# Kernel optimization log

Hardware: AMD Instinct MI355X
Metric: run time of the kernel (lower is better)

Reference implementation:

```python
import jax, jax.numpy as jnp
import numpy as np

B, N, H, NH = 2, 1024, 1024, 16  # batch, seq per branch, hidden, heads


def setup_inputs() -> dict:
    key = jax.random.key(0)
    k1, k2, k3, k4 = jax.random.split(key, 4)
    x = jax.random.normal(k1, (B, N, H), jnp.float32)
    x2 = jax.random.normal(k2, (B, N, H), jnp.float32)
    w_qkv = jax.random.normal(k3, (3 * H, H), jnp.float32) * 0.02  # nn.Linear(H, 3H), no bias
    w_out = jax.random.normal(k4, (H, H), jnp.float32) * 0.02
    b_out = jnp.zeros((H,), jnp.float32)
    return {"x": x, "x2": x2, "w_qkv": w_qkv, "w_out": w_out, "b_out": b_out, "num_heads": NH}


def _qkv_split(x, w_qkv, nh):
    # qkv Linear then Rearrange 'b n (qkv l d) -> qkv b l n d'
    b, n, h = x.shape
    d = h // nh
    qkv = x @ w_qkv.T                                    # [b, n, 3h]
    qkv = qkv.reshape(b, n, 3, nh, d).transpose(2, 0, 3, 1, 4)  # [3, b, nh, n, d]
    return qkv[0], qkv[1], qkv[2]


def reference(x, x2, w_qkv, w_out, b_out, num_heads):
    nh = num_heads
    d = x.shape[-1] // nh
    scale = float(d) ** -0.5
    q, k, v = _qkv_split(x, w_qkv, nh)
    q2, k2, v2 = _qkv_split(x2, w_qkv, nh)
    # cross-branch concat along seq dim
    q = jnp.concatenate([q, q2], axis=2)
    k = jnp.concatenate([k, k2], axis=2)
    v = jnp.concatenate([v, v2], axis=2)
    att = jax.nn.softmax(jnp.einsum('bhxd,bhyd->bhxy', q, k) * scale, axis=-1)  # [b,nh,2N,2N]
    o = jnp.einsum('bhxy,bhyd->bhxd', att, v)            # [b,nh,2N,d]
    o1, o2 = jnp.split(o, 2, axis=2)

    def proj(o):
        b, h, n, dd = o.shape
        o = o.transpose(0, 2, 1, 3).reshape(b, n, h * dd)  # 'b h l d -> b l (h d)'
        return o @ w_out.T + b_out

    return proj(o1), proj(o2)
```

## Files before the change

kernel.cpp:

```cpp
#include <hip/hip_runtime.h>
#include <hip/hip_bf16.h>

#define NB      2
#define NSEQ    1024
#define S2      2048
#define HDIM    1024
#define NHEADS  16
#define DHEAD   64
#define Q_SCALE 0.18033688011112042f

typedef unsigned short ushort_t;
typedef __attribute__((ext_vector_type(8))) short short8;
typedef __attribute__((ext_vector_type(4))) float f32x4;

__device__ __forceinline__ ushort_t f2bf(float f) {
    union { float f; unsigned int u; } c; c.f = f;
    unsigned int u = c.u;
    u += 0x7FFFu + ((u >> 16) & 1u);
    return (ushort_t)(u >> 16);
}

__device__ __forceinline__ unsigned pack_bf16x2(float a, float b) {
    union { __hip_bfloat162 h; unsigned u; } cv;
    cv.h = __float22bfloat162_rn(float2{a, b});
    return cv.u;
}

__global__ __launch_bounds__(256) void cvt_all(
    const float* __restrict__ x, const float* __restrict__ x2,
    const float* __restrict__ wqkv, const float* __restrict__ wout,
    ushort_t* __restrict__ Xb, ushort_t* __restrict__ Wqb, ushort_t* __restrict__ Wob)
{
    int b = blockIdx.x;
    const float* s; ushort_t* d; int i;
    if (b < 2048)      { s = x;    d = Xb;            i = b * 256 + threadIdx.x; }
    else if (b < 4096) { s = x2;   d = Xb + 2097152;  i = (b - 2048) * 256 + threadIdx.x; }
    else if (b < 7168) { s = wqkv; d = Wqb;           i = (b - 4096) * 256 + threadIdx.x; }
    else               { s = wout; d = Wob;           i = (b - 7168) * 256 + threadIdx.x; }
    float4 v = ((const float4*)s)[i];
    ushort4 o; o.x = f2bf(v.x); o.y = f2bf(v.y); o.z = f2bf(v.z); o.w = f2bf(v.w);
    ((ushort4*)d)[i] = o;
}

__global__ __launch_bounds__(256) void qkv_gemm_mfma(
    const ushort_t* __restrict__ Xb, const ushort_t* __restrict__ Wqb,
    ushort_t* __restrict__ Qb, ushort_t* __restrict__ Kb, ushort_t* __restrict__ Vtb)
{
    __shared__ ushort_t As[128 * 32];
    __shared__ ushort_t Bs[128 * 32];
    __shared__ float    Sc[4][16 * 20];
    const int t = threadIdx.x;
    const int lane = t & 63, quad = lane >> 4, l15 = lane & 15;
    const int w = t >> 6;
    const int wm = (w >> 1) * 64, wn = (w & 1) * 64;
    const int r0 = blockIdx.y * 128, c0 = blockIdx.x * 128;

    const int g_chunk = (lane & 3) ^ ((lane >> 3) & 3);
    const int srow_lo = w * 16 + (lane >> 2);

    f32x4 acc[4][4];
    #pragma unroll
    for (int i = 0; i < 4; ++i)
        #pragma unroll
        for (int j = 0; j < 4; ++j) acc[i][j] = (f32x4){0.f, 0.f, 0.f, 0.f};

    for (int k0 = 0; k0 < HDIM; k0 += 32) {
        __syncthreads();
        #pragma unroll
        for (int p = 0; p < 2; ++p) {
            int row = srow_lo + p * 64;
            const ushort_t* gpA = Xb  + (size_t)(r0 + row) * HDIM + k0 + g_chunk * 8;
            const ushort_t* gpB = Wqb + (size_t)(c0 + row) * HDIM + k0 + g_chunk * 8;
            ushort_t* lpA = As + p * 2048 + w * 512;
            ushort_t* lpB = Bs + p * 2048 + w * 512;
            __builtin_amdgcn_global_load_lds(
                (const __attribute__((address_space(1))) void*)gpA,
                (__attribute__((address_space(3))) void*)lpA, 16, 0, 0);
            __builtin_amdgcn_global_load_lds(
                (const __attribute__((address_space(1))) void*)gpB,
                (__attribute__((address_space(3))) void*)lpB, 16, 0, 0);
        }
        __syncthreads();
        const int sw = (l15 >> 1) & 3;
        short8 af[4], bf[4];
        #pragma unroll
        for (int mi = 0; mi < 4; ++mi) {
            int ra = wm + mi * 16 + l15;
            af[mi] = *(const short8*)(As + ra * 32 + ((quad ^ sw) * 8));
        }
        #pragma unroll
        for (int ni = 0; ni < 4; ++ni) {
            int rb = wn + ni * 16 + l15;
            bf[ni] = *(const short8*)(Bs + rb * 32 + ((quad ^ sw) * 8));
        }
        #pragma unroll
        for (int mi = 0; mi < 4; ++mi)
            #pragma unroll
            for (int ni = 0; ni < 4; ++ni)
                acc[mi][ni] = __builtin_amdgcn_mfma_f32_16x16x32_bf16(af[mi], bf[ni], acc[mi][ni], 0, 0, 0);
    }

    const int branch = r0 >> 11;
    const int bb     = (r0 & 2047) >> 10;
    const int qi     = c0 >> 10;
    float* sc = &Sc[w][0];

    if (qi == 2) {
        #pragma unroll
        for (int mi = 0; mi < 4; ++mi) {
            int sbase = branch * NSEQ + (r0 & 1023) + wm + mi * 16 + quad * 4;
            #pragma unroll
            for (int ni = 0; ni < 4; ++ni) {
                int cc = (c0 & 1023) + wn + ni * 16;
                int h  = cc >> 6;
                int dd = (cc & 63) + l15;
                ushort4 pv;
                pv.x = f2bf(acc[mi][ni][0]); pv.y = f2bf(acc[mi][ni][1]);
                pv.z = f2bf(acc[mi][ni][2]); pv.w = f2bf(acc[mi][ni][3]);
                *(ushort4*)(Vtb + ((size_t)(bb * NHEADS + h) * DHEAD + dd) * S2 + sbase) = pv;
            }
        }
    } else {
        const float qsc = (qi == 0) ? Q_SCALE : 1.0f;
        ushort_t* base = (qi ? Kb : Qb);
        const int row = lane >> 2, ch = lane & 3;
        #pragma unroll
        for (int mi = 0; mi < 4; ++mi) {
            int sb = branch * NSEQ + (r0 & 1023) + wm + mi * 16;
            #pragma unroll
            for (int ni = 0; ni < 4; ++ni) {
                int cc = (c0 & 1023) + wn + ni * 16;
                int h  = cc >> 6;
                int db = cc & 63;
                #pragma unroll
                for (int reg = 0; reg < 4; ++reg)
                    sc[(quad * 4 + reg) * 20 + l15] = acc[mi][ni][reg] * qsc;
                float4 v = *(const float4*)&sc[row * 20 + ch * 4];
                uint2 pk;
                pk.x = pack_bf16x2(v.x, v.y);
                pk.y = pack_bf16x2(v.z, v.w);
                *(uint2*)(base + ((size_t)(bb * NHEADS + h) * S2 + sb + row) * DHEAD + db + ch * 4) = pk;
            }
        }
    }
}

__global__ __launch_bounds__(256) void attn_mfma(
    const ushort_t* __restrict__ Qb, const ushort_t* __restrict__ Kb,
    const ushort_t* __restrict__ Vtb, ushort_t* __restrict__ Ob)
{
    __shared__ ushort_t Ks[2][64 * 64];
    __shared__ ushort_t Vs[2][64 * 64];
    __shared__ ushort_t Ps[64][72];

    const int t = threadIdx.x, lane = t & 63, quad = lane >> 4, l15 = lane & 15, w = t >> 6;
    const int bh = blockIdx.z * NHEADS + blockIdx.y;
    const int r0 = blockIdx.x * 128;
    const ushort_t* Qh  = Qb  + (size_t)bh * S2 * DHEAD;
    const ushort_t* Kh  = Kb  + (size_t)bh * S2 * DHEAD;
    const ushort_t* Vth = Vtb + (size_t)bh * DHEAD * S2;

    const int slot = lane & 7;
    const int rsub = lane >> 3;
    auto prefetch = [&](int kt_, int buf_) {
        #pragma unroll
        for (int c = 0; c < 2; ++c) {
            int row = w * 16 + c * 8 + rsub;
            int gK  = slot ^ ((row >> 2) & 7);
            int gV  = slot ^ (row & 7);
            const ushort_t* gpK = Kh  + (size_t)(kt_ * 64 + row) * DHEAD + gK * 8;
            const ushort_t* gpV = Vth + (size_t)row * S2 + kt_ * 64 + gV * 8;
            ushort_t* lpK = &Ks[buf_][w * 1024 + c * 512];
            ushort_t* lpV = &Vs[buf_][w * 1024 + c * 512];
            __builtin_amdgcn_global_load_lds(
                (const __attribute__((address_space(1))) void*)gpK,
                (__attribute__((address_space(3))) void*)lpK, 16, 0, 0);
            __builtin_amdgcn_global_load_lds(
                (const __attribute__((address_space(1))) void*)gpV,
                (__attribute__((address_space(3))) void*)lpV, 16, 0, 0);
        }
    };

    short8 aq[2][2];
    #pragma unroll
    for (int s = 0; s < 2; ++s) {
        const int qrow = r0 + 32 * w + 16 * s + l15;
        aq[s][0] = *(const short8*)(Qh + (size_t)qrow * DHEAD + quad * 8);
        aq[s][1] = *(const short8*)(Qh + (size_t)qrow * DHEAD + 32 + quad * 8);
    }

    float lacc[2][4] = {};
    f32x4 oacc[2][4];
    #pragma unroll
    for (int s = 0; s < 2; ++s)
        #pragma unroll
        for (int nt = 0; nt < 4; ++nt) oacc[s][nt] = (f32x4){0.f, 0.f, 0.f, 0.f};

    prefetch(0, 0);
    prefetch(1, 1);
    __syncthreads();

    for (int kt = 0; kt < S2 / 64; ++kt) {
        const ushort_t* kb = &Ks[kt & 1][0];
        const ushort_t* vb = &Vs[kt & 1][0];

        short8 kf[4][2];
        #pragma unroll
        for (int nt = 0; nt < 4; ++nt) {
            const int key = 4 * l15 + nt;
            const ushort_t* krow = kb + key * 64;
            const int swz = l15 & 7;
            kf[nt][0] = *(const short8*)(krow + ((quad       ^ swz) * 8));
            kf[nt][1] = *(const short8*)(krow + (((4 + quad) ^ swz) * 8));
        }

        f32x4 sacc[2][4];
        #pragma unroll
        for (int s = 0; s < 2; ++s)
            #pragma unroll
            for (int nt = 0; nt < 4; ++nt) {
                f32x4 sv = (f32x4){0.f, 0.f, 0.f, 0.f};
                sv = __builtin_amdgcn_mfma_f32_16x16x32_bf16(aq[s][0], kf[nt][0], sv, 0, 0, 0);
                sv = __builtin_amdgcn_mfma_f32_16x16x32_bf16(aq[s][1], kf[nt][1], sv, 0, 0, 0);
                sacc[s][nt] = sv;
            }

        short8 vf[4][2];
        #pragma unroll
        for (int nt = 0; nt < 4; ++nt) {
            const int drow = nt * 16 + l15;
            vf[nt][0] = *(const short8*)(vb + drow * 64 + ((quad       ^ (drow & 7)) * 8));
            vf[nt][1] = *(const short8*)(vb + drow * 64 + (((4 + quad) ^ (drow & 7)) * 8));
        }

        #pragma unroll
        for (int s = 0; s < 2; ++s) {
            #pragma unroll
            for (int reg = 0; reg < 4; ++reg) {
                float p0 = __builtin_exp2f(sacc[s][0][reg]);
                float p1 = __builtin_exp2f(sacc[s][1][reg]);
                float p2 = __builtin_exp2f(sacc[s][2][reg]);
                float p3 = __builtin_exp2f(sacc[s][3][reg]);
                lacc[s][reg] += (p0 + p1) + (p2 + p3);
                uint2 pk;
                pk.x = pack_bf16x2(p0, p1);
                pk.y = pack_bf16x2(p2, p3);
                int prow = 16 * w + quad * 4 + reg;
                *(uint2*)&Ps[prow][4 * l15] = pk;
            }
            #pragma unroll
            for (int kk = 0; kk < 2; ++kk) {
                short8 pa = *(const short8*)&Ps[16 * w + l15][kk * 32 + quad * 8];
                #pragma unroll
                for (int nt = 0; nt < 4; ++nt)
                    oacc[s][nt] = __builtin_amdgcn_mfma_f32_16x16x32_bf16(pa, vf[nt][kk], oacc[s][nt], 0, 0, 0);
            }
        }

        __syncthreads();
        if (kt + 2 < S2 / 64) prefetch(kt + 2, kt & 1);
    }

    #pragma unroll
    for (int s = 0; s < 2; ++s)
        #pragma unroll
        for (int reg = 0; reg < 4; ++reg) {
            float l = lacc[s][reg];
            l += __shfl_xor(l, 1);
            l += __shfl_xor(l, 2);
            l += __shfl_xor(l, 4);
            l += __shfl_xor(l, 8);
            float inv = 1.f / l;
            size_t rowoff = ((size_t)bh * S2 + r0 + 32 * w + 16 * s + quad * 4 + reg) * DHEAD;
            #pragma unroll
            for (int nt = 0; nt < 4; ++nt)
                Ob[rowoff + nt * 16 + l15] = f2bf(oacc[s][nt][reg] * inv);
        }
}

__global__ __launch_bounds__(256) void proj_gemm_mfma(
    const ushort_t* __restrict__ Ob, const ushort_t* __restrict__ Wob,
    const float* __restrict__ Bo, float* __restrict__ Out)
{
    __shared__ ushort_t As[128 * 32];
    __shared__ ushort_t Bs[64 * 32];
    __shared__ float    Sc[4][16 * 20];
    const int t = threadIdx.x;
    const int lane = t & 63, quad = lane >> 4, l15 = lane & 15;
    const int w = t >> 6;
    const int wm = (w >> 1) * 64, wn = (w & 1) * 32;
    const int r0 = blockIdx.y * 128, c0 = blockIdx.x * 64;
    const int branch = r0 >> 11, bb = (r0 & 2047) >> 10;

    const int g_chunk = (lane & 3) ^ ((lane >> 3) & 3);
    const int srow_lo = w * 16 + (lane >> 2);

    f32x4 acc[4][2];
    #pragma unroll
    for (int i = 0; i < 4; ++i)
        #pragma unroll
        for (int j = 0; j < 2; ++j) acc[i][j] = (f32x4){0.f, 0.f, 0.f, 0.f};

    for (int k0 = 0; k0 < HDIM; k0 += 32) {
        int h = k0 >> 6, off = k0 & 63;
        __syncthreads();
        {
            const ushort_t* gpB = Wob + (size_t)(c0 + srow_lo) * HDIM + k0 + g_chunk * 8;
            ushort_t* lpB = Bs + w * 512;
            __builtin_amdgcn_global_load_lds(
                (const __attribute__((address_space(1))) void*)gpB,
                (__attribute__((address_space(3))) void*)lpB, 16, 0, 0);
        }
        #pragma unroll
        for (int p = 0; p < 2; ++p) {
            int row = srow_lo + p * 64;
            int s = branch * NSEQ + (r0 & 1023) + row;
            const ushort_t* gpA = Ob + ((size_t)(bb * NHEADS + h) * S2 + s) * DHEAD + off + g_chunk * 8;
            ushort_t* lpA = As + p * 2048 + w * 512;
            __builtin_amdgcn_global_load_lds(
                (const __attribute__((address_space(1))) void*)gpA,
                (__attribute__((address_space(3))) void*)lpA, 16, 0, 0);
        }
        __syncthreads();
        const int sw = (l15 >> 1) & 3;
        short8 af[4], bf[2];
        #pragma unroll
        for (int mi = 0; mi < 4; ++mi) {
            int ra = wm + mi * 16 + l15;
            af[mi] = *(const short8*)(As + ra * 32 + ((quad ^ sw) * 8));
        }
        #pragma unroll
        for (int ni = 0; ni < 2; ++ni) {
            int rb = wn + ni * 16 + l15;
            bf[ni] = *(const short8*)(Bs + rb * 32 + ((quad ^ sw) * 8));
        }
        #pragma unroll
        for (int mi = 0; mi < 4; ++mi)
            #pragma unroll
            for (int ni = 0; ni < 2; ++ni)
                acc[mi][ni] = __builtin_amdgcn_mfma_f32_16x16x32_bf16(af[mi], bf[ni], acc[mi][ni], 0, 0, 0);
    }

    float* sc = &Sc[w][0];
    const int row = lane >> 2, ch = lane & 3;
    #pragma unroll
    for (int mi = 0; mi < 4; ++mi) {
        int rb0 = r0 + wm + mi * 16;
        #pragma unroll
        for (int ni = 0; ni < 2; ++ni) {
            int cb = c0 + wn + ni * 16;
            #pragma unroll
            for (int reg = 0; reg < 4; ++reg)
                sc[(quad * 4 + reg) * 20 + l15] = acc[mi][ni][reg];
            float4 v = *(const float4*)&sc[row * 20 + ch * 4];
            float4 bias = *(const float4*)&Bo[cb + ch * 4];
            v.x += bias.x; v.y += bias.y; v.z += bias.z; v.w += bias.w;
            *(float4*)&Out[(size_t)(rb0 + row) * HDIM + cb + ch * 4] = v;
        }
    }
}

extern "C" void kernel_launch(void* const* d_in, const int* in_sizes, int n_in,
                              void* d_out, int out_size, void* d_ws, size_t ws_size,
                              hipStream_t stream) {
    const float* x    = (const float*)d_in[0];
    const float* x2   = (const float*)d_in[1];
    const float* wqkv = (const float*)d_in[2];
    const float* wout = (const float*)d_in[3];
    const float* bout = (const float*)d_in[4];
    float* out = (float*)d_out;

    char* ws = (char*)d_ws;
    ushort_t* Xb  = (ushort_t*)(ws);
    ushort_t* Wqb = (ushort_t*)(ws + (8u  << 20));
    ushort_t* Wob = (ushort_t*)(ws + (14u << 20));
    ushort_t* Qb  = (ushort_t*)(ws + (16u << 20));
    ushort_t* Kb  = (ushort_t*)(ws + (24u << 20));
    ushort_t* Vtb = (ushort_t*)(ws + (32u << 20));
    ushort_t* Ob  = (ushort_t*)(ws + (40u << 20));

    cvt_all<<<8192, 256, 0, stream>>>(x, x2, wqkv, wout, Xb, Wqb, Wob);
    qkv_gemm_mfma<<<dim3(24, 32), 256, 0, stream>>>(Xb, Wqb, Qb, Kb, Vtb);
    attn_mfma<<<dim3(S2 / 128, NHEADS, NB), 256, 0, stream>>>(Qb, Kb, Vtb, Ob);
    proj_gemm_mfma<<<dim3(16, 32), 256, 0, stream>>>(Ob, Wob, bout, out);
}
```

Before: 224.6 us.

## Double-buffer LDS tiles in QKV and output projection GEMMs

Both bf16 MFMA GEMM kernels now keep two LDS buffers for the A and B tiles. They prefetch the k-tile two steps ahead with global_load_lds after the compute of the current step. This is meant to overlap global-to-LDS transfers with MFMA work and cut the loop to one barrier per iteration instead of two. In exchange it doubles LDS usage per block, which may reduce occupancy, and it relies on the barrier draining earlier asynchronous loads.

New measurement: 212.5 us. 1.06x faster.

```diff
diff --git a/kernel.cpp b/kernel.cpp
--- a/kernel.cpp
+++ b/kernel.cpp
@@ -46,8 +46,8 @@
     const ushort_t* __restrict__ Xb, const ushort_t* __restrict__ Wqb,
     ushort_t* __restrict__ Qb, ushort_t* __restrict__ Kb, ushort_t* __restrict__ Vtb)
 {
-    __shared__ ushort_t As[128 * 32];
-    __shared__ ushort_t Bs[128 * 32];
+    __shared__ ushort_t As[2 * 128 * 32];
+    __shared__ ushort_t Bs[2 * 128 * 32];
     __shared__ float    Sc[4][16 * 20];
     const int t = threadIdx.x;
     const int lane = t & 63, quad = lane >> 4, l15 = lane & 15;
@@ -58,21 +58,14 @@
     const int g_chunk = (lane & 3) ^ ((lane >> 3) & 3);
     const int srow_lo = w * 16 + (lane >> 2);
 
-    f32x4 acc[4][4];
-    #pragma unroll
-    for (int i = 0; i < 4; ++i)
-        #pragma unroll
-        for (int j = 0; j < 4; ++j) acc[i][j] = (f32x4){0.f, 0.f, 0.f, 0.f};
-
-    for (int k0 = 0; k0 < HDIM; k0 += 32) {
-        __syncthreads();
+    auto stage = [&](int k0, int buf) {
         #pragma unroll
         for (int p = 0; p < 2; ++p) {
             int row = srow_lo + p * 64;
             const ushort_t* gpA = Xb  + (size_t)(r0 + row) * HDIM + k0 + g_chunk * 8;
             const ushort_t* gpB = Wqb + (size_t)(c0 + row) * HDIM + k0 + g_chunk * 8;
-            ushort_t* lpA = As + p * 2048 + w * 512;
-            ushort_t* lpB = Bs + p * 2048 + w * 512;
+            ushort_t* lpA = As + buf * 4096 + p * 2048 + w * 512;
+            ushort_t* lpB = Bs + buf * 4096 + p * 2048 + w * 512;
             __builtin_amdgcn_global_load_lds(
                 (const __attribute__((address_space(1))) void*)gpA,
                 (__attribute__((address_space(3))) void*)lpA, 16, 0, 0);
@@ -80,24 +73,40 @@
                 (const __attribute__((address_space(1))) void*)gpB,
                 (__attribute__((address_space(3))) void*)lpB, 16, 0, 0);
         }
-        __syncthreads();
-        const int sw = (l15 >> 1) & 3;
+    };
+
+    f32x4 acc[4][4];
+    #pragma unroll
+    for (int i = 0; i < 4; ++i)
+        #pragma unroll
+        for (int j = 0; j < 4; ++j) acc[i][j] = (f32x4){0.f, 0.f, 0.f, 0.f};
+
+    stage(0, 0);
+    stage(32, 1);
+    __syncthreads();
+
+    const int sw = (l15 >> 1) & 3;
+    for (int it = 0; it < 32; ++it) {
+        const ushort_t* a = As + (it & 1) * 4096;
+        const ushort_t* b = Bs + (it & 1) * 4096;
         short8 af[4], bf[4];
         #pragma unroll
         for (int mi = 0; mi < 4; ++mi) {
             int ra = wm + mi * 16 + l15;
-            af[mi] = *(const short8*)(As + ra * 32 + ((quad ^ sw) * 8));
+            af[mi] = *(const short8*)(a + ra * 32 + ((quad ^ sw) * 8));
         }
         #pragma unroll
         for (int ni = 0; ni < 4; ++ni) {
             int rb = wn + ni * 16 + l15;
-            bf[ni] = *(const short8*)(Bs + rb * 32 + ((quad ^ sw) * 8));
+            bf[ni] = *(const short8*)(b + rb * 32 + ((quad ^ sw) * 8));
         }
         #pragma unroll
         for (int mi = 0; mi < 4; ++mi)
             #pragma unroll
             for (int ni = 0; ni < 4; ++ni)
                 acc[mi][ni] = __builtin_amdgcn_mfma_f32_16x16x32_bf16(af[mi], bf[ni], acc[mi][ni], 0, 0, 0);
+        __syncthreads();
+        if (it < 30) stage((it + 2) * 32, it & 1);
     }
 
     const int branch = r0 >> 11;
@@ -282,8 +291,8 @@
     const ushort_t* __restrict__ Ob, const ushort_t* __restrict__ Wob,
     const float* __restrict__ Bo, float* __restrict__ Out)
 {
-    __shared__ ushort_t As[128 * 32];
-    __shared__ ushort_t Bs[64 * 32];
+    __shared__ ushort_t As[2 * 128 * 32];
+    __shared__ ushort_t Bs[2 * 64 * 32];
     __shared__ float    Sc[4][16 * 20];
     const int t = threadIdx.x;
     const int lane = t & 63, quad = lane >> 4, l15 = lane & 15;
@@ -295,50 +304,57 @@
     const int g_chunk = (lane & 3) ^ ((lane >> 3) & 3);
     const int srow_lo = w * 16 + (lane >> 2);
 
-    f32x4 acc[4][2];
-    #pragma unroll
-    for (int i = 0; i < 4; ++i)
-        #pragma unroll
-        for (int j = 0; j < 2; ++j) acc[i][j] = (f32x4){0.f, 0.f, 0.f, 0.f};
-
-    for (int k0 = 0; k0 < HDIM; k0 += 32) {
+    auto stage = [&](int k0, int buf) {
         int h = k0 >> 6, off = k0 & 63;
-        __syncthreads();
-        {
-            const ushort_t* gpB = Wob + (size_t)(c0 + srow_lo) * HDIM + k0 + g_chunk * 8;
-            ushort_t* lpB = Bs + w * 512;
-            __builtin_amdgcn_global_load_lds(
-                (const __attribute__((address_space(1))) void*)gpB,
-                (__attribute__((address_space(3))) void*)lpB, 16, 0, 0);
-        }
+        const ushort_t* gpB = Wob + (size_t)(c0 + srow_lo) * HDIM + k0 + g_chunk * 8;
+        ushort_t* lpB = Bs + buf * 2048 + w * 512;
+        __builtin_amdgcn_global_load_lds(
+            (const __attribute__((address_space(1))) void*)gpB,
+            (__attribute__((address_space(3))) void*)lpB, 16, 0, 0);
         #pragma unroll
         for (int p = 0; p < 2; ++p) {
             int row = srow_lo + p * 64;
             int s = branch * NSEQ + (r0 & 1023) + row;
             const ushort_t* gpA = Ob + ((size_t)(bb * NHEADS + h) * S2 + s) * DHEAD + off + g_chunk * 8;
-            ushort_t* lpA = As + p * 2048 + w * 512;
+            ushort_t* lpA = As + buf * 4096 + p * 2048 + w * 512;
             __builtin_amdgcn_global_load_lds(
                 (const __attribute__((address_space(1))) void*)gpA,
                 (__attribute__((address_space(3))) void*)lpA, 16, 0, 0);
         }
-        __syncthreads();
-        const int sw = (l15 >> 1) & 3;
+    };
+
+    f32x4 acc[4][2];
+    #pragma unroll
+    for (int i = 0; i < 4; ++i)
+        #pragma unroll
+        for (int j = 0; j < 2; ++j) acc[i][j] = (f32x4){0.f, 0.f, 0.f, 0.f};
+
+    stage(0, 0);
+    stage(32, 1);
+    __syncthreads();
+
+    const int sw = (l15 >> 1) & 3;
+    for (int it = 0; it < 32; ++it) {
+        const ushort_t* a = As + (it & 1) * 4096;
+        const ushort_t* b = Bs + (it & 1) * 2048;
         short8 af[4], bf[2];
         #pragma unroll
         for (int mi = 0; mi < 4; ++mi) {
             int ra = wm + mi * 16 + l15;
-            af[mi] = *(const short8*)(As + ra * 32 + ((quad ^ sw) * 8));
+            af[mi] = *(const short8*)(a + ra * 32 + ((quad ^ sw) * 8));
         }
         #pragma unroll
         for (int ni = 0; ni < 2; ++ni) {
             int rb = wn + ni * 16 + l15;
-            bf[ni] = *(const short8*)(Bs + rb * 32 + ((quad ^ sw) * 8));
+            bf[ni] = *(const short8*)(b + rb * 32 + ((quad ^ sw) * 8));
         }
         #pragma unroll
         for (int mi = 0; mi < 4; ++mi)
             #pragma unroll
             for (int ni = 0; ni < 2; ++ni)
                 acc[mi][ni] = __builtin_amdgcn_mfma_f32_16x16x32_bf16(af[mi], bf[ni], acc[mi][ni], 0, 0, 0);
+        __syncthreads();
+        if (it < 30) stage((it + 2) * 32, it & 1);
     }
 
     float* sc = &Sc[w][0];
```
